# Performance work log

Hardware: AMD Instinct MI355X
Metric: run time of the kernel (lower is better)

The kernel has to match this reference:

```python
import jax, jax.numpy as jnp
import numpy as np

QMIN, QMAX = -128.0, 127.0          # int-8 symmetric range
CONST_N = 15.0                      # shift-exp range constant
OUT_BIT = 8                         # const_output_bit
INT32_MAX = 2.0 ** 31 - 1.0


def setup_inputs() -> dict:
    key = jax.random.key(0)
    kx, ks = jax.random.split(key)
    x = jax.random.normal(kx, (4, 2048, 4096), dtype=jnp.float32)
    # per-channel quantizer scale ~ abs-max / 127 statistics
    scaler = jnp.max(jnp.abs(x), axis=(0, 1)) / 127.0 + 1e-6  # [D]
    return {"x": x, "scaler": scaler}


def _int_exp_shift(x_int, sf):
    # x_int ~ integer-valued float tensor; sf per-channel scaling factor [D]
    x_int = x_int + jnp.floor(x_int / 2.0) - jnp.floor(x_int / 16.0)  # *1.4375 ~ /ln2
    x0 = jnp.floor(-1.0 / sf)                     # [D], negative
    x_int = jnp.maximum(x_int, CONST_N * x0)
    q = jnp.floor(x_int / x0)
    r = x_int - x0 * q
    e = r / 2.0 - x0
    return jnp.maximum(jnp.floor(e * jnp.exp2(CONST_N - q)), 0.0)


def reference(x, scaler):
    # quantize input per-channel (int8 grid, kept in float)
    pre_x_int = jnp.clip(jnp.round(x / scaler), QMIN, QMAX)
    sf_sig = scaler * 1.702

    x_int_max = jnp.max(pre_x_int, axis=-1, keepdims=True)   # [B,S,1]
    x_int = pre_x_int - x_int_max

    exp_int = _int_exp_shift(x_int, sf_sig)                  # [B,S,D]
    exp_int_max = _int_exp_shift(-x_int_max, sf_sig)         # [B,S,D] (bcast)
    exp_sum = jnp.minimum(exp_int + exp_int_max, INT32_MAX)

    factor = jnp.floor(INT32_MAX / exp_sum)
    sigmoid_int = jnp.floor(exp_int * factor / 2.0 ** (31 - OUT_BIT + 1))

    sigmoid_scale = 1.0 / 2.0 ** (OUT_BIT - 1)    # 1/128
    y = pre_x_int * sigmoid_int * (scaler * sigmoid_scale)
    return y
```

## Files before the change

kernel.cpp:

```cpp
#include <hip/hip_runtime.h>


#define D 4096
#define BLK 512
#define CPT 8
#define RPB 8
#define NW (BLK / 64)
#define NSLOT 16
#define TENT (NSLOT * 256)
#define EPS 1e-4f
#define F2_31 2147483648.0f

typedef float f32x4 __attribute__((ext_vector_type(4)));

__device__ __forceinline__ float exp_fast(float xi, float nx0, float rx0) {
    const float q = floorf(fmaf(xi, rx0, EPS));
    const float r = fmaf(nx0, q, xi);
    const float e = fmaf(r, 0.5f, nx0);
    return floorf(ldexpf(e, 15 - (int)q));
}

__device__ __forceinline__ float exp_slow(float xi, float x0) {
    xi = fmaxf(xi, 15.0f * x0);
    const float q = floorf(xi / x0);
    const float r = fmaf(-x0, q, xi);
    const float e = fmaf(r, 0.5f, -x0);
    return fmaxf(floorf(e * ldexpf(1.0f, 15 - (int)q)), 0.0f);
}

__global__ __launch_bounds__(BLK) void quantgelu_kernel(
    const float* __restrict__ x, const float* __restrict__ scaler,
    float* __restrict__ out, int nrows)
{
    const int tid  = threadIdx.x;
    const int wid  = tid >> 6;
    const int lane = tid & 63;
    const int row0 = blockIdx.x * RPB;

    __shared__ __align__(16) float sred[2][NW];
    __shared__ __align__(16) float smax[NW];
    __shared__ float eit[TENT];
    __shared__ float sigt[TENT];

    float s_[CPT], rs_[CPT], s128_[CPT], x0_[CPT];
    #pragma unroll
    for (int k = 0; k < CPT / 4; ++k) {
        const int col = k * (BLK * 4) + tid * 4;
        const float4 sv = *reinterpret_cast<const float4*>(scaler + col);
        const float ss[4] = {sv.x, sv.y, sv.z, sv.w};
        #pragma unroll
        for (int j = 0; j < 4; ++j) {
            const int i = k * 4 + j;
            const float s = ss[j];
            s_[i]    = s;
            rs_[i]   = 1.0f / s;
            s128_[i] = s * 0.0078125f;
            x0_[i]   = floorf(-1.0f / (s * 1.702f));
        }
    }

    long long base = (long long)row0 * D;
    float4 xv[CPT / 4];
    if (row0 < nrows) {
        #pragma unroll
        for (int k = 0; k < CPT / 4; ++k)
            xv[k] = *reinterpret_cast<const float4*>(x + base + k * (BLK * 4) + tid * 4);
    }

    float x0mn = x0_[0], x0mx = x0_[0];
    #pragma unroll
    for (int i = 1; i < CPT; ++i) {
        x0mn = fminf(x0mn, x0_[i]);
        x0mx = fmaxf(x0mx, x0_[i]);
    }
    #pragma unroll
    for (int off = 1; off < 64; off <<= 1) {
        x0mn = fminf(x0mn, __shfl_xor(x0mn, off));
        x0mx = fmaxf(x0mx, __shfl_xor(x0mx, off));
    }
    if ((tid & 63) == 0) { sred[0][wid] = x0mn; sred[1][wid] = x0mx; }
    __syncthreads();
    #pragma unroll
    for (int w = 0; w < NW; ++w) {
        x0mn = fminf(x0mn, sred[0][w]);
        x0mx = fmaxf(x0mx, sred[1][w]);
    }

    const int  nslots = (int)(x0mx - x0mn) + 1;
    const bool ok = (x0mn >= -64.0f) && (nslots <= NSLOT);
    const int  nent = nslots << 8;

    int bo_[CPT];
    #pragma unroll
    for (int i = 0; i < CPT; ++i)
        bo_[i] = ((int)(x0_[i] - x0mn)) << 8;

    const float x0l  = x0mn + (float)lane;
    const float nx0l = -x0l;
    const float rx0l = 1.0f / x0l;
    const float c15l = 15.0f * x0l;

    if (ok) {
        for (int e = tid; e < nent; e += BLK) {
            const int   slot = e >> 8;
            const float x0v  = x0mn + (float)slot;
            float xi = -(float)(e & 255);
            xi = xi + floorf(xi * 0.5f) - floorf(xi * 0.0625f);
            xi = fmaxf(xi, 15.0f * x0v);
            eit[e] = exp_fast(xi, -x0v, __shfl(rx0l, slot));
        }
    }

    for (int r = 0; r < RPB; ++r) {
        const int row = row0 + r;
        if (row >= nrows) break;

        float4 xn[CPT / 4];
        if (r + 1 < RPB && row + 1 < nrows) {
            #pragma unroll
            for (int k = 0; k < CPT / 4; ++k)
                xn[k] = *reinterpret_cast<const float4*>(x + base + D + k * (BLK * 4) + tid * 4);
        }

        float pre[CPT];
        float vmax = -INFINITY;
        const float* xf = reinterpret_cast<const float*>(xv);
        #pragma unroll
        for (int i = 0; i < CPT; ++i) {
            const float q0 = xf[i] * rs_[i];
            const float rr = fmaf(-s_[i], q0, xf[i]);
            const float qq = fmaf(rr, rs_[i], q0);
            float p = rintf(qq);
            p = fminf(fmaxf(p, -128.0f), 127.0f);
            pre[i] = p;
            vmax = fmaxf(vmax, p);
        }
        #pragma unroll
        for (int off = 1; off < 64; off <<= 1)
            vmax = fmaxf(vmax, __shfl_xor(vmax, off));
        if ((tid & 63) == 0) smax[wid] = vmax;
        __syncthreads();
        {
            const float4 a = *reinterpret_cast<const float4*>(smax);
            const float4 b = *reinterpret_cast<const float4*>(smax + 4);
            vmax = fmaxf(fmaxf(fmaxf(a.x, a.y), fmaxf(a.z, a.w)),
                         fmaxf(fmaxf(b.x, b.y), fmaxf(b.z, b.w)));
        }

        const float xm  = -vmax;
        const float xmt = xm + floorf(xm * 0.5f) - floorf(xm * 0.0625f);

        float res[CPT];
        if (ok) {
            const float em_l = exp_fast(fmaxf(xmt, c15l), nx0l, rx0l);

            for (int e = tid; e < nent; e += BLK) {
                const int   slot = e >> 8;
                const float em   = __shfl(em_l, slot);
                const float ei   = eit[e];
                const float esum   = fminf(ei + em, F2_31);
                const float factor = floorf(F2_31 / esum);
                sigt[e] = floorf((ei * factor) * 0x1p-24f);
            }
            __syncthreads();

            #pragma unroll
            for (int i = 0; i < CPT; ++i) {
                const int d = (int)(vmax - pre[i]);
                res[i] = (pre[i] * sigt[bo_[i] + d]) * s128_[i];
            }
        } else {
            #pragma unroll
            for (int i = 0; i < CPT; ++i) {
                const float x0 = x0_[i];
                float xi = pre[i] - vmax;
                xi = xi + floorf(xi * 0.5f) - floorf(xi * 0.0625f);
                const float ei = exp_slow(xi, x0);
                const float em = exp_slow(xmt, x0);
                const float esum   = fminf(ei + em, F2_31);
                const float factor = floorf(F2_31 / esum);
                const float sig    = floorf((ei * factor) * 0x1p-24f);
                res[i] = (pre[i] * sig) * s128_[i];
            }
        }

        #pragma unroll
        for (int k = 0; k < CPT / 4; ++k) {
            f32x4 ov;
            ov.x = res[k * 4 + 0]; ov.y = res[k * 4 + 1];
            ov.z = res[k * 4 + 2]; ov.w = res[k * 4 + 3];
            __builtin_nontemporal_store(
                ov, reinterpret_cast<f32x4*>(out + base + k * (BLK * 4) + tid * 4));
        }

        base += D;
        #pragma unroll
        for (int k = 0; k < CPT / 4; ++k) xv[k] = xn[k];
    }
}

extern "C" void kernel_launch(void* const* d_in, const int* in_sizes, int n_in,
                              void* d_out, int out_size, void* d_ws, size_t ws_size,
                              hipStream_t stream) {
    const float* x      = (const float*)d_in[0];
    const float* scaler = (const float*)d_in[1];
    float* out          = (float*)d_out;

    const int nrows = in_sizes[0] / D;
    const int grid  = (nrows + RPB - 1) / RPB;
    quantgelu_kernel<<<grid, BLK, 0, stream>>>(x, scaler, out, nrows);
}
```

Measured before the change: 48.73 us.

## Process two rows per iteration with paired reductions and packed int8 state

The row loop now handles two rows at a time. It does a combined block max reduction, builds two sigmoid lookup tables (siga/sigb) and needs one barrier per row pair, so barriers and loop overhead are roughly halved. Quantized values and slot indices are packed into bytes to cut register pressure. It also adds a launch-bounds occupancy hint, shrinks NSLOT to 12 to reduce shared memory, and folds the 1/128 scale into the table. The risks are a narrower range of channel scales that can use the fast table path, more shared memory for two tables, and an extra barrier added in the setup.

Measured after the change: 111.9 us. 2.3x slower.

```diff
diff --git a/kernel.cpp b/kernel.cpp
--- a/kernel.cpp
+++ b/kernel.cpp
@@ -6,7 +6,7 @@
 #define CPT 8
 #define RPB 8
 #define NW (BLK / 64)
-#define NSLOT 16
+#define NSLOT 12
 #define TENT (NSLOT * 256)
 #define EPS 1e-4f
 #define F2_31 2147483648.0f
@@ -28,7 +28,7 @@
     return fmaxf(floorf(e * ldexpf(1.0f, 15 - (int)q)), 0.0f);
 }
 
-__global__ __launch_bounds__(BLK) void quantgelu_kernel(
+__global__ __launch_bounds__(BLK, 8) void quantgelu_kernel(
     const float* __restrict__ x, const float* __restrict__ scaler,
     float* __restrict__ out, int nrows)
 {
@@ -37,34 +37,38 @@
     const int lane = tid & 63;
     const int row0 = blockIdx.x * RPB;
 
-    __shared__ __align__(16) float sred[2][NW];
-    __shared__ __align__(16) float smax[NW];
+    __shared__ __align__(16) float smax2[2][NW];
     __shared__ float eit[TENT];
-    __shared__ float sigt[TENT];
-
-    float s_[CPT], rs_[CPT], s128_[CPT], x0_[CPT];
-    #pragma unroll
-    for (int k = 0; k < CPT / 4; ++k) {
-        const int col = k * (BLK * 4) + tid * 4;
-        const float4 sv = *reinterpret_cast<const float4*>(scaler + col);
+    __shared__ float siga[TENT];
+    __shared__ float sigb[TENT];
+
+    const int c0 = tid * 4;
+    const int c1 = BLK * 4 + tid * 4;
+
+    long long base = (long long)row0 * D;
+    float4 xv[4] = {};
+    if (row0 < nrows) {
+        xv[0] = *reinterpret_cast<const float4*>(x + base + c0);
+        xv[1] = *reinterpret_cast<const float4*>(x + base + c1);
+    }
+    if (row0 + 1 < nrows) {
+        xv[2] = *reinterpret_cast<const float4*>(x + base + D + c0);
+        xv[3] = *reinterpret_cast<const float4*>(x + base + D + c1);
+    }
+
+    float s_[CPT], rs_[CPT], x0_[CPT];
+    #pragma unroll
+    for (int k = 0; k < 2; ++k) {
+        const float4 sv = *reinterpret_cast<const float4*>(scaler + (k ? c1 : c0));
         const float ss[4] = {sv.x, sv.y, sv.z, sv.w};
         #pragma unroll
         for (int j = 0; j < 4; ++j) {
             const int i = k * 4 + j;
             const float s = ss[j];
-            s_[i]    = s;
-            rs_[i]   = 1.0f / s;
-            s128_[i] = s * 0.0078125f;
-            x0_[i]   = floorf(-1.0f / (s * 1.702f));
-        }
-    }
-
-    long long base = (long long)row0 * D;
-    float4 xv[CPT / 4];
-    if (row0 < nrows) {
-        #pragma unroll
-        for (int k = 0; k < CPT / 4; ++k)
-            xv[k] = *reinterpret_cast<const float4*>(x + base + k * (BLK * 4) + tid * 4);
+            s_[i]  = s;
+            rs_[i] = 1.0f / s;
+            x0_[i] = floorf(-1.0f / (s * 1.702f));
+        }
     }
 
     float x0mn = x0_[0], x0mx = x0_[0];
@@ -78,22 +82,27 @@
         x0mn = fminf(x0mn, __shfl_xor(x0mn, off));
         x0mx = fmaxf(x0mx, __shfl_xor(x0mx, off));
     }
-    if ((tid & 63) == 0) { sred[0][wid] = x0mn; sred[1][wid] = x0mx; }
+    if (lane == 0) { smax2[0][wid] = x0mn; smax2[1][wid] = x0mx; }
     __syncthreads();
     #pragma unroll
     for (int w = 0; w < NW; ++w) {
-        x0mn = fminf(x0mn, sred[0][w]);
-        x0mx = fmaxf(x0mx, sred[1][w]);
-    }
+        x0mn = fminf(x0mn, smax2[0][w]);
+        x0mx = fmaxf(x0mx, smax2[1][w]);
+    }
+    __syncthreads();
 
     const int  nslots = (int)(x0mx - x0mn) + 1;
     const bool ok = (x0mn >= -64.0f) && (nslots <= NSLOT);
     const int  nent = nslots << 8;
 
-    int bo_[CPT];
-    #pragma unroll
-    for (int i = 0; i < CPT; ++i)
-        bo_[i] = ((int)(x0_[i] - x0mn)) << 8;
+    unsigned slotpk[2] = {0u, 0u};
+    #pragma unroll
+    for (int k = 0; k < 2; ++k)
+        #pragma unroll
+        for (int j = 0; j < 4; ++j) {
+            const float sl = fminf(fmaxf(x0_[k * 4 + j] - x0mn, 0.0f), 255.0f);
+            slotpk[k] |= ((unsigned)(int)sl & 0xffu) << (8 * j);
+        }
 
     const float x0l  = x0mn + (float)lane;
     const float nx0l = -x0l;
@@ -111,91 +120,163 @@
         }
     }
 
-    for (int r = 0; r < RPB; ++r) {
-        const int row = row0 + r;
-        if (row >= nrows) break;
-
-        float4 xn[CPT / 4];
-        if (r + 1 < RPB && row + 1 < nrows) {
+    for (int g = 0; g < RPB / 2; ++g) {
+        const int ra = row0 + 2 * g;
+        if (ra >= nrows) break;
+        const bool bval = (ra + 1) < nrows;
+
+        float va = -INFINITY, vb = -INFINITY;
+        unsigned pk[4] = {0u, 0u, 0u, 0u};
+        #pragma unroll
+        for (int k = 0; k < 2; ++k) {
+            const float* xa = reinterpret_cast<const float*>(&xv[k]);
+            const float* xb = reinterpret_cast<const float*>(&xv[2 + k]);
             #pragma unroll
-            for (int k = 0; k < CPT / 4; ++k)
-                xn[k] = *reinterpret_cast<const float4*>(x + base + D + k * (BLK * 4) + tid * 4);
-        }
-
-        float pre[CPT];
-        float vmax = -INFINITY;
-        const float* xf = reinterpret_cast<const float*>(xv);
-        #pragma unroll
-        for (int i = 0; i < CPT; ++i) {
-            const float q0 = xf[i] * rs_[i];
-            const float rr = fmaf(-s_[i], q0, xf[i]);
-            const float qq = fmaf(rr, rs_[i], q0);
-            float p = rintf(qq);
-            p = fminf(fmaxf(p, -128.0f), 127.0f);
-            pre[i] = p;
-            vmax = fmaxf(vmax, p);
-        }
-        #pragma unroll
-        for (int off = 1; off < 64; off <<= 1)
-            vmax = fmaxf(vmax, __shfl_xor(vmax, off));
-        if ((tid & 63) == 0) smax[wid] = vmax;
+            for (int j = 0; j < 4; ++j) {
+                const int i = k * 4 + j;
+                float q0 = xa[j] * rs_[i];
+                float rr = fmaf(-s_[i], q0, xa[j]);
+                float p  = __builtin_amdgcn_fmed3f(
+                               rintf(fmaf(rr, rs_[i], q0)), -128.0f, 127.0f);
+                va = fmaxf(va, p);
+                pk[k] |= ((unsigned)(int)p & 0xffu) << (8 * j);
+
+                q0 = xb[j] * rs_[i];
+                rr = fmaf(-s_[i], q0, xb[j]);
+                p  = __builtin_amdgcn_fmed3f(
+                               rintf(fmaf(rr, rs_[i], q0)), -128.0f, 127.0f);
+                vb = fmaxf(vb, p);
+                pk[2 + k] |= ((unsigned)(int)p & 0xffu) << (8 * j);
+            }
+        }
+
+        {
+            const long long nb = base + 2 * D;
+            if (ra + 2 < nrows) {
+                xv[0] = *reinterpret_cast<const float4*>(x + nb + c0);
+                xv[1] = *reinterpret_cast<const float4*>(x + nb + c1);
+            }
+            if (ra + 3 < nrows) {
+                xv[2] = *reinterpret_cast<const float4*>(x + nb + D + c0);
+                xv[3] = *reinterpret_cast<const float4*>(x + nb + D + c1);
+            }
+        }
+
+        #pragma unroll
+        for (int off = 1; off < 64; off <<= 1) {
+            va = fmaxf(va, __shfl_xor(va, off));
+            vb = fmaxf(vb, __shfl_xor(vb, off));
+        }
+        if (lane == 0) { smax2[0][wid] = va; smax2[1][wid] = vb; }
         __syncthreads();
         {
-            const float4 a = *reinterpret_cast<const float4*>(smax);
-            const float4 b = *reinterpret_cast<const float4*>(smax + 4);
-            vmax = fmaxf(fmaxf(fmaxf(a.x, a.y), fmaxf(a.z, a.w)),
-                         fmaxf(fmaxf(b.x, b.y), fmaxf(b.z, b.w)));
-        }
-
-        const float xm  = -vmax;
-        const float xmt = xm + floorf(xm * 0.5f) - floorf(xm * 0.0625f);
-
-        float res[CPT];
+            const float4 a0 = *reinterpret_cast<const float4*>(&smax2[0][0]);
+            const float4 a1 = *reinterpret_cast<const float4*>(&smax2[0][4]);
+            const float4 b0 = *reinterpret_cast<const float4*>(&smax2[1][0]);
+            const float4 b1 = *reinterpret_cast<const float4*>(&smax2[1][4]);
+            va = fmaxf(fmaxf(fmaxf(a0.x, a0.y), fmaxf(a0.z, a0.w)),
+                       fmaxf(fmaxf(a1.x, a1.y), fmaxf(a1.z, a1.w)));
+            vb = fmaxf(fmaxf(fmaxf(b0.x, b0.y), fmaxf(b0.z, b0.w)),
+                       fmaxf(fmaxf(b1.x, b1.y), fmaxf(b1.z, b1.w)));
+        }
+
+        const float xma  = -va, xmb = -vb;
+        const float xmta = xma + floorf(xma * 0.5f) - floorf(xma * 0.0625f);
+        const float xmtb = xmb + floorf(xmb * 0.5f) - floorf(xmb * 0.0625f);
+
         if (ok) {
-            const float em_l = exp_fast(fmaxf(xmt, c15l), nx0l, rx0l);
-
+            const float em_al = exp_fast(fmaxf(xmta, c15l), nx0l, rx0l);
+            const float em_bl = exp_fast(fmaxf(xmtb, c15l), nx0l, rx0l);
             for (int e = tid; e < nent; e += BLK) {
-                const int   slot = e >> 8;
-                const float em   = __shfl(em_l, slot);
-                const float ei   = eit[e];
+                const float ei     = eit[e];
+                const float em     = __shfl(em_al, e >> 8);
                 const float esum   = fminf(ei + em, F2_31);
                 const float factor = floorf(F2_31 / esum);
-                sigt[e] = floorf((ei * factor) * 0x1p-24f);
-            }
-            __syncthreads();
-
+                siga[e] = floorf((ei * factor) * 0x1p-24f) * 0.0078125f;
+            }
+            if (bval) {
+                for (int e = tid; e < nent; e += BLK) {
+                    const float ei     = eit[e];
+                    const float em     = __shfl(em_bl, e >> 8);
+                    const float esum   = fminf(ei + em, F2_31);
+                    const float factor = floorf(F2_31 / esum);
+                    sigb[e] = floorf((ei * factor) * 0x1p-24f) * 0.0078125f;
+                }
+            }
+        }
+        __syncthreads();
+
+        if (ok) {
+            const int via = (int)va, vib = (int)vb;
             #pragma unroll
-            for (int i = 0; i < CPT; ++i) {
-                const int d = (int)(vmax - pre[i]);
-                res[i] = (pre[i] * sigt[bo_[i] + d]) * s128_[i];
+            for (int k = 0; k < 2; ++k) {
+                f32x4 ov;
+                #pragma unroll
+                for (int j = 0; j < 4; ++j) {
+                    const int pi   = (int)(signed char)((pk[k] >> (8 * j)) & 0xffu);
+                    const int slot = (int)((slotpk[k] >> (8 * j)) & 0xffu);
+                    const float sg = siga[(slot << 8) + (via - pi)];
+                    ov[j] = ((float)pi * sg) * s_[k * 4 + j];
+                }
+                __builtin_nontemporal_store(
+                    ov, reinterpret_cast<f32x4*>(out + base + (k ? c1 : c0)));
+            }
+            if (bval) {
+                #pragma unroll
+                for (int k = 0; k < 2; ++k) {
+                    f32x4 ov;
+                    #pragma unroll
+                    for (int j = 0; j < 4; ++j) {
+                        const int pi   = (int)(signed char)((pk[2 + k] >> (8 * j)) & 0xffu);
+                        const int slot = (int)((slotpk[k] >> (8 * j)) & 0xffu);
+                        const float sg = sigb[(slot << 8) + (vib - pi)];
+                        ov[j] = ((float)pi * sg) * s_[k * 4 + j];
+                    }
+                    __builtin_nontemporal_store(
+                        ov, reinterpret_cast<f32x4*>(out + base + D + (k ? c1 : c0)));
+                }
             }
         } else {
             #pragma unroll
-            for (int i = 0; i < CPT; ++i) {
-                const float x0 = x0_[i];
-                float xi = pre[i] - vmax;
-                xi = xi + floorf(xi * 0.5f) - floorf(xi * 0.0625f);
-                const float ei = exp_slow(xi, x0);
-                const float em = exp_slow(xmt, x0);
-                const float esum   = fminf(ei + em, F2_31);
-                const float factor = floorf(F2_31 / esum);
-                const float sig    = floorf((ei * factor) * 0x1p-24f);
-                res[i] = (pre[i] * sig) * s128_[i];
-            }
-        }
-
-        #pragma unroll
-        for (int k = 0; k < CPT / 4; ++k) {
-            f32x4 ov;
-            ov.x = res[k * 4 + 0]; ov.y = res[k * 4 + 1];
-            ov.z = res[k * 4 + 2]; ov.w = res[k * 4 + 3];
-            __builtin_nontemporal_store(
-                ov, reinterpret_cast<f32x4*>(out + base + k * (BLK * 4) + tid * 4));
-        }
-
-        base += D;
-        #pragma unroll
-        for (int k = 0; k < CPT / 4; ++k) xv[k] = xn[k];
+            for (int k = 0; k < 2; ++k) {
+                f32x4 ov, ow;
+                #pragma unroll
+                for (int j = 0; j < 4; ++j) {
+                    const int i = k * 4 + j;
+                    const float x0 = floorf(-1.0f / (s_[i] * 1.702f));
+                    const float s128 = s_[i] * 0.0078125f;
+                    {
+                        const float p = (float)(int)(signed char)((pk[k] >> (8 * j)) & 0xffu);
+                        float xi = p - va;
+                        xi = xi + floorf(xi * 0.5f) - floorf(xi * 0.0625f);
+                        const float ei = exp_slow(xi, x0);
+                        const float em = exp_slow(xmta, x0);
+                        const float esum   = fminf(ei + em, F2_31);
+                        const float factor = floorf(F2_31 / esum);
+                        const float sig    = floorf((ei * factor) * 0x1p-24f);
+                        ov[j] = (p * sig) * s128;
+                    }
+                    {
+                        const float p = (float)(int)(signed char)((pk[2 + k] >> (8 * j)) & 0xffu);
+                        float xi = p - vb;
+                        xi = xi + floorf(xi * 0.5f) - floorf(xi * 0.0625f);
+                        const float ei = exp_slow(xi, x0);
+                        const float em = exp_slow(xmtb, x0);
+                        const float esum   = fminf(ei + em, F2_31);
+                        const float factor = floorf(F2_31 / esum);
+                        const float sig    = floorf((ei * factor) * 0x1p-24f);
+                        ow[j] = (p * sig) * s128;
+                    }
+                }
+                __builtin_nontemporal_store(
+                    ov, reinterpret_cast<f32x4*>(out + base + (k ? c1 : c0)));
+                if (bval)
+                    __builtin_nontemporal_store(
+                        ow, reinterpret_cast<f32x4*>(out + base + D + (k ? c1 : c0)));
+            }
+        }
+
+        base += 2 * D;
     }
 }
 
```

## Batch row max reductions and build per-row sigmoid tables in one pass

Applied to the files above, without the earlier changes.

Each block now handles 4 rows instead of 8. It quantizes all of them up front, keeping the int8 values packed into registers, and does the max reductions for every row before a single barrier. It then builds a sigmoid lookup table per row in one fused pass, with no separate exp table, and writes all outputs after a second barrier. This replaces the per-row barrier-plus-table-rebuild sequence, cutting synchronisations and the shared-memory round trips. In exchange, shared memory per block grows, the grid doubles, and channels whose slot falls outside the table drop to a per-element slow path.

Result: slower. 52.88 us (+8.5%).

```diff
diff --git a/kernel.cpp b/kernel.cpp
--- a/kernel.cpp
+++ b/kernel.cpp
@@ -4,10 +4,9 @@
 #define D 4096
 #define BLK 512
 #define CPT 8
-#define RPB 8
+#define RPB 4
 #define NW (BLK / 64)
-#define NSLOT 16
-#define TENT (NSLOT * 256)
+#define NSLOT 9
 #define EPS 1e-4f
 #define F2_31 2147483648.0f
 
@@ -37,165 +36,177 @@
     const int lane = tid & 63;
     const int row0 = blockIdx.x * RPB;
 
+    __shared__ float sigt[RPB][NSLOT * 256];
+    __shared__ __align__(16) float smax[RPB][NW];
     __shared__ __align__(16) float sred[2][NW];
-    __shared__ __align__(16) float smax[NW];
-    __shared__ float eit[TENT];
-    __shared__ float sigt[TENT];
-
-    float s_[CPT], rs_[CPT], s128_[CPT], x0_[CPT];
-    #pragma unroll
-    for (int k = 0; k < CPT / 4; ++k) {
-        const int col = k * (BLK * 4) + tid * 4;
-        const float4 sv = *reinterpret_cast<const float4*>(scaler + col);
-        const float ss[4] = {sv.x, sv.y, sv.z, sv.w};
-        #pragma unroll
-        for (int j = 0; j < 4; ++j) {
-            const int i = k * 4 + j;
-            const float s = ss[j];
-            s_[i]    = s;
-            rs_[i]   = 1.0f / s;
-            s128_[i] = s * 0.0078125f;
-            x0_[i]   = floorf(-1.0f / (s * 1.702f));
-        }
-    }
-
-    long long base = (long long)row0 * D;
-    float4 xv[CPT / 4];
-    if (row0 < nrows) {
-        #pragma unroll
-        for (int k = 0; k < CPT / 4; ++k)
-            xv[k] = *reinterpret_cast<const float4*>(x + base + k * (BLK * 4) + tid * 4);
-    }
-
-    float x0mn = x0_[0], x0mx = x0_[0];
-    #pragma unroll
-    for (int i = 1; i < CPT; ++i) {
-        x0mn = fminf(x0mn, x0_[i]);
-        x0mx = fmaxf(x0mx, x0_[i]);
-    }
-    #pragma unroll
-    for (int off = 1; off < 64; off <<= 1) {
-        x0mn = fminf(x0mn, __shfl_xor(x0mn, off));
-        x0mx = fmaxf(x0mx, __shfl_xor(x0mx, off));
-    }
-    if ((tid & 63) == 0) { sred[0][wid] = x0mn; sred[1][wid] = x0mx; }
+
+    const int c0 = tid * 4;
+    const int c1 = BLK * 4 + tid * 4;
+
+    long long rb[RPB];
+    #pragma unroll
+    for (int r = 0; r < RPB; ++r)
+        rb[r] = (long long)(row0 + r < nrows ? row0 + r : nrows - 1) * D;
+
+    float4 xv[4];
+    xv[0] = *reinterpret_cast<const float4*>(x + rb[0] + c0);
+    xv[1] = *reinterpret_cast<const float4*>(x + rb[0] + c1);
+    xv[2] = *reinterpret_cast<const float4*>(x + rb[1] + c0);
+    xv[3] = *reinterpret_cast<const float4*>(x + rb[1] + c1);
+
+    float s_[CPT], rs_[CPT];
+    float x0mn, x0mx;
+    {
+        float mn = 1.0f, mx = -1e30f;
+        #pragma unroll
+        for (int k = 0; k < 2; ++k) {
+            const float4 sv = *reinterpret_cast<const float4*>(scaler + (k ? c1 : c0));
+            const float ss[4] = {sv.x, sv.y, sv.z, sv.w};
+            #pragma unroll
+            for (int j = 0; j < 4; ++j) {
+                const int i = k * 4 + j;
+                const float s = ss[j];
+                s_[i]  = s;
+                rs_[i] = 1.0f / s;
+                const float x0 = floorf(-1.0f / (s * 1.702f));
+                mn = fminf(mn, x0);
+                mx = fmaxf(mx, x0);
+            }
+        }
+        #pragma unroll
+        for (int off = 1; off < 64; off <<= 1) {
+            mn = fminf(mn, __shfl_xor(mn, off));
+            mx = fmaxf(mx, __shfl_xor(mx, off));
+        }
+        if (lane == 0) { sred[0][wid] = mn; sred[1][wid] = mx; }
+        x0mn = mn; x0mx = mx;
+    }
+
+    unsigned pk[2 * RPB];
+    #pragma unroll
+    for (int r = 0; r < RPB; ++r) {
+        const int p = (r & 1) * 2;
+        float vmax = -INFINITY;
+        unsigned pk0 = 0u, pk1 = 0u;
+        #pragma unroll
+        for (int k = 0; k < 2; ++k) {
+            const float* xa = reinterpret_cast<const float*>(&xv[p + k]);
+            #pragma unroll
+            for (int j = 0; j < 4; ++j) {
+                const int i = k * 4 + j;
+                const float q0 = xa[j] * rs_[i];
+                const float rr = fmaf(-s_[i], q0, xa[j]);
+                const float pv = __builtin_amdgcn_fmed3f(
+                                    rintf(fmaf(rr, rs_[i], q0)), -128.0f, 127.0f);
+                vmax = fmaxf(vmax, pv);
+                const unsigned b = ((unsigned)(int)pv & 0xffu) << (8 * j);
+                if (k == 0) pk0 |= b; else pk1 |= b;
+            }
+        }
+        pk[2 * r]     = pk0;
+        pk[2 * r + 1] = pk1;
+        if (r + 2 < RPB) {
+            xv[p]     = *reinterpret_cast<const float4*>(x + rb[r + 2] + c0);
+            xv[p + 1] = *reinterpret_cast<const float4*>(x + rb[r + 2] + c1);
+        }
+        #pragma unroll
+        for (int off = 1; off < 64; off <<= 1)
+            vmax = fmaxf(vmax, __shfl_xor(vmax, off));
+        if (lane == 0) smax[r][wid] = vmax;
+    }
+
     __syncthreads();
+
     #pragma unroll
     for (int w = 0; w < NW; ++w) {
         x0mn = fminf(x0mn, sred[0][w]);
         x0mx = fmaxf(x0mx, sred[1][w]);
     }
-
-    const int  nslots = (int)(x0mx - x0mn) + 1;
-    const bool ok = (x0mn >= -64.0f) && (nslots <= NSLOT);
-    const int  nent = nslots << 8;
-
-    int bo_[CPT];
-    #pragma unroll
-    for (int i = 0; i < CPT; ++i)
-        bo_[i] = ((int)(x0_[i] - x0mn)) << 8;
-
-    const float x0l  = x0mn + (float)lane;
-    const float nx0l = -x0l;
-    const float rx0l = 1.0f / x0l;
-    const float c15l = 15.0f * x0l;
-
-    if (ok) {
+    const int nsl = (int)(x0mx - x0mn) + 1;
+    const int tb  = nsl < NSLOT ? nsl : NSLOT;
+
+    unsigned slotpk[2] = {0u, 0u};
+    #pragma unroll
+    for (int k = 0; k < 2; ++k)
+        #pragma unroll
+        for (int j = 0; j < 4; ++j) {
+            const float x0 = floorf(-1.0f / (s_[k * 4 + j] * 1.702f));
+            const int   sl = (int)(x0 - x0mn);
+            const unsigned byte = (x0 >= -64.0f && sl < tb) ? (unsigned)sl : 255u;
+            slotpk[k] |= (byte & 0xffu) << (8 * j);
+        }
+
+    int   vmaxi[RPB];
+    float xmt_[RPB];
+    #pragma unroll
+    for (int r = 0; r < RPB; ++r) {
+        const float4 a = *reinterpret_cast<const float4*>(&smax[r][0]);
+        const float4 b = *reinterpret_cast<const float4*>(&smax[r][4]);
+        const float vm = fmaxf(fmaxf(fmaxf(a.x, a.y), fmaxf(a.z, a.w)),
+                               fmaxf(fmaxf(b.x, b.y), fmaxf(b.z, b.w)));
+        vmaxi[r] = (int)vm;
+        const float xm = -vm;
+        xmt_[r] = xm + floorf(xm * 0.5f) - floorf(xm * 0.0625f);
+    }
+
+    {
+        const float x0l  = x0mn + (float)lane;
+        const float nx0l = -x0l;
+        const float rx0l = 1.0f / x0l;
+        const float c15l = 15.0f * x0l;
+        float em_l[RPB];
+        #pragma unroll
+        for (int r = 0; r < RPB; ++r)
+            em_l[r] = exp_fast(fmaxf(xmt_[r], c15l), nx0l, rx0l);
+
+        const int nent = tb << 8;
         for (int e = tid; e < nent; e += BLK) {
             const int   slot = e >> 8;
             const float x0v  = x0mn + (float)slot;
+            const float rx0v = __shfl(rx0l, slot);
             float xi = -(float)(e & 255);
             xi = xi + floorf(xi * 0.5f) - floorf(xi * 0.0625f);
             xi = fmaxf(xi, 15.0f * x0v);
-            eit[e] = exp_fast(xi, -x0v, __shfl(rx0l, slot));
-        }
-    }
-
+            const float ei = exp_fast(xi, -x0v, rx0v);
+            #pragma unroll
+            for (int r = 0; r < RPB; ++r) {
+                const float em = __shfl(em_l[r], slot);
+                const float f  = floorf(F2_31 / fminf(ei + em, F2_31));
+                sigt[r][e] = floorf((ei * f) * 0x1p-24f) * 0.0078125f;
+            }
+        }
+    }
+    __syncthreads();
+
+    #pragma unroll
     for (int r = 0; r < RPB; ++r) {
-        const int row = row0 + r;
-        if (row >= nrows) break;
-
-        float4 xn[CPT / 4];
-        if (r + 1 < RPB && row + 1 < nrows) {
-            #pragma unroll
-            for (int k = 0; k < CPT / 4; ++k)
-                xn[k] = *reinterpret_cast<const float4*>(x + base + D + k * (BLK * 4) + tid * 4);
-        }
-
-        float pre[CPT];
-        float vmax = -INFINITY;
-        const float* xf = reinterpret_cast<const float*>(xv);
-        #pragma unroll
-        for (int i = 0; i < CPT; ++i) {
-            const float q0 = xf[i] * rs_[i];
-            const float rr = fmaf(-s_[i], q0, xf[i]);
-            const float qq = fmaf(rr, rs_[i], q0);
-            float p = rintf(qq);
-            p = fminf(fmaxf(p, -128.0f), 127.0f);
-            pre[i] = p;
-            vmax = fmaxf(vmax, p);
-        }
-        #pragma unroll
-        for (int off = 1; off < 64; off <<= 1)
-            vmax = fmaxf(vmax, __shfl_xor(vmax, off));
-        if ((tid & 63) == 0) smax[wid] = vmax;
-        __syncthreads();
-        {
-            const float4 a = *reinterpret_cast<const float4*>(smax);
-            const float4 b = *reinterpret_cast<const float4*>(smax + 4);
-            vmax = fmaxf(fmaxf(fmaxf(a.x, a.y), fmaxf(a.z, a.w)),
-                         fmaxf(fmaxf(b.x, b.y), fmaxf(b.z, b.w)));
-        }
-
-        const float xm  = -vmax;
-        const float xmt = xm + floorf(xm * 0.5f) - floorf(xm * 0.0625f);
-
-        float res[CPT];
-        if (ok) {
-            const float em_l = exp_fast(fmaxf(xmt, c15l), nx0l, rx0l);
-
-            for (int e = tid; e < nent; e += BLK) {
-                const int   slot = e >> 8;
-                const float em   = __shfl(em_l, slot);
-                const float ei   = eit[e];
-                const float esum   = fminf(ei + em, F2_31);
-                const float factor = floorf(F2_31 / esum);
-                sigt[e] = floorf((ei * factor) * 0x1p-24f);
-            }
-            __syncthreads();
-
-            #pragma unroll
-            for (int i = 0; i < CPT; ++i) {
-                const int d = (int)(vmax - pre[i]);
-                res[i] = (pre[i] * sigt[bo_[i] + d]) * s128_[i];
-            }
-        } else {
-            #pragma unroll
-            for (int i = 0; i < CPT; ++i) {
-                const float x0 = x0_[i];
-                float xi = pre[i] - vmax;
-                xi = xi + floorf(xi * 0.5f) - floorf(xi * 0.0625f);
-                const float ei = exp_slow(xi, x0);
-                const float em = exp_slow(xmt, x0);
-                const float esum   = fminf(ei + em, F2_31);
-                const float factor = floorf(F2_31 / esum);
-                const float sig    = floorf((ei * factor) * 0x1p-24f);
-                res[i] = (pre[i] * sig) * s128_[i];
-            }
-        }
-
-        #pragma unroll
-        for (int k = 0; k < CPT / 4; ++k) {
+        if (row0 + r >= nrows) break;
+        #pragma unroll
+        for (int k = 0; k < 2; ++k) {
             f32x4 ov;
-            ov.x = res[k * 4 + 0]; ov.y = res[k * 4 + 1];
-            ov.z = res[k * 4 + 2]; ov.w = res[k * 4 + 3];
+            #pragma unroll
+            for (int j = 0; j < 4; ++j) {
+                const int i  = k * 4 + j;
+                const int pi = (int)(signed char)((pk[2 * r + k] >> (8 * j)) & 0xffu);
+                const unsigned sb = (slotpk[k] >> (8 * j)) & 0xffu;
+                if (sb != 255u) {
+                    const float sg = sigt[r][((int)sb << 8) + (vmaxi[r] - pi)];
+                    ov[j] = ((float)pi * sg) * s_[i];
+                } else {
+                    const float x0 = floorf(-1.0f / (s_[i] * 1.702f));
+                    const float pf = (float)pi;
+                    float xi = pf - (float)vmaxi[r];
+                    xi = xi + floorf(xi * 0.5f) - floorf(xi * 0.0625f);
+                    const float ei = exp_slow(xi, x0);
+                    const float em = exp_slow(xmt_[r], x0);
+                    const float factor = floorf(F2_31 / fminf(ei + em, F2_31));
+                    ov[j] = (pf * floorf((ei * factor) * 0x1p-24f))
+                            * (s_[i] * 0.0078125f);
+                }
+            }
             __builtin_nontemporal_store(
-                ov, reinterpret_cast<f32x4*>(out + base + k * (BLK * 4) + tid * 4));
-        }
-
-        base += D;
-        #pragma unroll
-        for (int k = 0; k < CPT / 4; ++k) xv[k] = xn[k];
+                ov, reinterpret_cast<f32x4*>(out + rb[r] + (k ? c1 : c0)));
+        }
     }
 }
 
```
